# Optimization experiments

Hardware: AMD Instinct MI355X
Metric: run time of the kernel (lower is better)

The kernel has to match this reference:

```python
import jax, jax.numpy as jnp
import numpy as np

LATENT_DIM = 256
BOOK_SIZE = 8192


def setup_inputs() -> dict:
    key = jax.random.key(0)
    k1, k2 = jax.random.split(key)
    z_e = jax.random.normal(k1, (16, LATENT_DIM, 32, 32), dtype=jnp.float32)
    codebook = jax.random.normal(k2, (BOOK_SIZE, LATENT_DIM), dtype=jnp.float32)
    return {"z_e": z_e, "codebook": codebook}


def reference(z_e, codebook):
    # NCHW -> NHWC -> (B*H*W, D)
    flat_z = jnp.transpose(z_e, (0, 2, 3, 1)).reshape(-1, LATENT_DIM)
    # squared euclidean distance via matmul: ||z||^2 + ||e||^2 - 2 z.e
    dist = (
        jnp.sum(flat_z ** 2, axis=1, keepdims=True)
        + jnp.sum(codebook ** 2, axis=1)
        - 2.0 * flat_z @ codebook.T
    )  # (N, book_size)
    indices = jnp.argmin(dist, axis=1)          # (N,)
    z_q = codebook[indices]                      # (N, D) gather
    return z_q, indices
```

## Files before the change

### kernel.cpp

```cpp
#include <hip/hip_runtime.h>
#include <stdint.h>

#define NROWS 16384
#define NCODES 8192
#define DIM 256
#define EPS_S 0.4f
#define SM 0.5f

typedef __attribute__((ext_vector_type(8))) short bf16x8;
typedef __attribute__((ext_vector_type(16))) float f32x16;
typedef unsigned int uint32;

__device__ __forceinline__ unsigned short f2bf(float f) {
  union { float f; unsigned int u; } v; v.f = f;
  unsigned int u = v.u;
  return (unsigned short)((u + 0x7FFFu + ((u >> 16) & 1u)) >> 16);
}

__device__ __forceinline__ unsigned long long packdi(float d, int idx) {
  unsigned int u = __float_as_uint(d);
  u = (u & 0x80000000u) ? ~u : (u | 0x80000000u);
  return ((unsigned long long)u << 32) | (unsigned int)idx;
}
__device__ __forceinline__ unsigned long long u64min(unsigned long long a,
                                                     unsigned long long b) {
  return a < b ? a : b;
}
__device__ __forceinline__ unsigned long long shflx64(unsigned long long v, int m) {
  int lo = __shfl_xor((int)(unsigned int)v, m);
  int hi = __shfl_xor((int)(v >> 32), m);
  return ((unsigned long long)(unsigned int)hi << 32) | (unsigned int)lo;
}
__device__ __forceinline__ uint32 umax(uint32 a, uint32 b) { return a > b ? a : b; }
__device__ __forceinline__ uint32 umin(uint32 a, uint32 b) { return a < b ? a : b; }

__device__ __forceinline__ void glds16(const ushort* g, ushort* l) {
  __builtin_amdgcn_global_load_lds(
      (const __attribute__((address_space(1))) unsigned int*)g,
      (__attribute__((address_space(3))) unsigned int*)l, 16, 0, 0);
}

__global__ __launch_bounds__(256) void prep(const float* __restrict__ z,
                                            const float* __restrict__ cb,
                                            float* __restrict__ flatz,
                                            ushort* __restrict__ zb,
                                            ushort* __restrict__ eb,
                                            float* __restrict__ enorm) {
  __shared__ float t[32][33];
  const int blk = blockIdx.x;
  if (blk < 4096) {
    const int tx = threadIdx.x & 31, ty = threadIdx.x >> 5;
    const int ht = blk & 31, ct = (blk >> 5) & 7, b = blk >> 8;
    const float* src = z + (size_t)b * 262144 + (size_t)(ct * 32) * 1024 + ht * 32;
#pragma unroll
    for (int i = 0; i < 4; ++i) {
      int c = ty + i * 8;
      t[c][tx] = src[c * 1024 + tx];
    }
    __syncthreads();
    const int r = threadIdx.x >> 3, q = threadIdx.x & 7;
    float4 vv;
    vv.x = t[q * 4 + 0][r];
    vv.y = t[q * 4 + 1][r];
    vv.z = t[q * 4 + 2][r];
    vv.w = t[q * 4 + 3][r];
    const int row = b * 1024 + ht * 32 + r;
    *(float4*)(flatz + (size_t)row * 256 + ct * 32 + q * 4) = vv;
    ushort4 o;
    o.x = f2bf(vv.x); o.y = f2bf(vv.y); o.z = f2bf(vv.z); o.w = f2bf(vv.w);
    *(ushort4*)(zb + (size_t)row * 256 + ct * 32 + q * 4) = o;
  } else {
    const int lane = threadIdx.x & 63, wave = threadIdx.x >> 6;
    const int code = (blk - 4096) * 4 + wave;
    float4 v = *(const float4*)(cb + (size_t)code * 256 + lane * 4);
    ushort4 o;
    o.x = f2bf(v.x); o.y = f2bf(v.y); o.z = f2bf(v.z); o.w = f2bf(v.w);
    *(ushort4*)(eb + (size_t)code * 256 + lane * 4) = o;
    float ss = v.x * v.x + v.y * v.y + v.z * v.z + v.w * v.w;
#pragma unroll
    for (int s = 1; s < 64; s <<= 1) ss += __shfl_xor(ss, s);
    if (lane == 0) enorm[code] = ss;
  }
}

__device__ __forceinline__ void init_acc(f32x16 acc[4][2], const float* en,
                                         int ot, int wm, int lg) {
#pragma unroll
  for (int m = 0; m < 4; ++m) {
    const float* ep = en + ot * 256 + wm * 128 + m * 32 + 4 * lg;
    float4 e0 = *(const float4*)(ep);
    float4 e1 = *(const float4*)(ep + 8);
    float4 e2 = *(const float4*)(ep + 16);
    float4 e3 = *(const float4*)(ep + 24);
    f32x16 c0;
    c0[0]  = 1024.f - 0.5f * e0.x; c0[1]  = 1024.f - 0.5f * e0.y;
    c0[2]  = 1024.f - 0.5f * e0.z; c0[3]  = 1024.f - 0.5f * e0.w;
    c0[4]  = 1024.f - 0.5f * e1.x; c0[5]  = 1024.f - 0.5f * e1.y;
    c0[6]  = 1024.f - 0.5f * e1.z; c0[7]  = 1024.f - 0.5f * e1.w;
    c0[8]  = 1024.f - 0.5f * e2.x; c0[9]  = 1024.f - 0.5f * e2.y;
    c0[10] = 1024.f - 0.5f * e2.z; c0[11] = 1024.f - 0.5f * e2.w;
    c0[12] = 1024.f - 0.5f * e3.x; c0[13] = 1024.f - 0.5f * e3.y;
    c0[14] = 1024.f - 0.5f * e3.z; c0[15] = 1024.f - 0.5f * e3.w;
    acc[m][0] = c0; acc[m][1] = c0;
  }
}

__device__ __forceinline__ void epilogue(const f32x16 acc[4][2],
                                         uint32* __restrict__ bm, int cg,
                                         int ot, int zrow0, int wm, int wn,
                                         int l31, int lg) {
  const int cid0 = cg * 128 + ot * 16 + wm * 8;
#pragma unroll
  for (int n = 0; n < 2; ++n) {
    uint32 res[8];
#pragma unroll
    for (int m = 0; m < 4; ++m)
#pragma unroll
      for (int hc = 0; hc < 2; ++hc) {
        uint32 m1 = 0, m2 = 0;
#pragma unroll
        for (int p = 0; p < 8; ++p) {
          uint32 id = (uint32)((p & 3) | (lg << 2) | ((p >> 2) << 3));
          uint32 pv = (__float_as_uint(acc[m][n][hc * 8 + p]) & ~31u) | id;
          m2 = umax(m2, umin(m1, pv));
          m1 = umax(m1, pv);
        }
        uint32 o1 = (uint32)__shfl_xor((int)m1, 32);
        uint32 o2 = (uint32)__shfl_xor((int)m2, 32);
        m2 = umax(umax(m2, o2), umin(m1, o1));
        m1 = umax(m1, o1);
        float s1 = __uint_as_float(m1 & ~31u);
        float s2 = __uint_as_float(m2 & ~31u);
        res[m * 2 + hc] = (s1 - s2 > SM) ? (m1 | 16u) : m1;
      }
    const int zr = zrow0 + wn * 64 + n * 32 + l31;
    uint4 o;
    o.x = lg ? res[4] : res[0];
    o.y = lg ? res[5] : res[1];
    o.z = lg ? res[6] : res[2];
    o.w = lg ? res[7] : res[3];
    *(uint4*)(bm + (size_t)zr * 512 + cid0 + lg * 4) = o;
  }
}

__global__ __launch_bounds__(512, 2) void vq_gemm(const ushort* __restrict__ eb,
                                                  const ushort* __restrict__ zb,
                                                  const float* __restrict__ enorm,
                                                  uint32* __restrict__ bm) {
  __shared__ __align__(16) ushort As[4 * 8192];
  __shared__ __align__(16) ushort Bs[4 * 8192];
  __shared__ __align__(16) float en[2048];
  const int tid = threadIdx.x;
  const int wave = tid >> 6, lane = tid & 63;
  const int wm = wave >> 2, wn = wave & 3;
  const int l31 = lane & 31, lg = lane >> 5;
  const int y = blockIdx.x & 63, cg = blockIdx.x >> 6;
  const int code00 = cg * 2048;
  const int zrow0 = y * 256;

  *(float4*)&en[tid * 4] = *(const float4*)(enorm + code00 + tid * 4);
  __syncthreads();

  const int u0 = tid, u1 = tid + 512;
  const ushort* aU0 = eb + (size_t)(code00 + (u0 >> 2)) * 256 +
                      ((u0 & 3) ^ ((u0 >> 3) & 3)) * 8;
  const ushort* aU1 = eb + (size_t)(code00 + (u1 >> 2)) * 256 +
                      ((u1 & 3) ^ ((u1 >> 3) & 3)) * 8;
  const ushort* bU0 = zb + (size_t)(zrow0 + (u0 >> 2)) * 256 +
                      ((u0 & 3) ^ ((u0 >> 3) & 3)) * 8;
  const ushort* bU1 = zb + (size_t)(zrow0 + (u1 >> 2)) * 256 +
                      ((u1 & 3) ^ ((u1 >> 3) & 3)) * 8;
  ushort* aL = As + wave * 512;
  ushort* bL = Bs + wave * 512;

#pragma unroll
  for (int c = 0; c < 3; ++c) {
    glds16(aU0 + c * 32, aL + c * 8192);
    glds16(aU1 + c * 32, aL + c * 8192 + 4096);
    glds16(bU0 + c * 32, bL + c * 8192);
    glds16(bU1 + c * 32, bL + c * 8192 + 4096);
  }

  f32x16 acc[4][2];
  init_acc(acc, en, 0, wm, lg);

  asm volatile("s_waitcnt vmcnt(8)" ::: "memory");
  __builtin_amdgcn_s_barrier();
  asm volatile("" ::: "memory");

  const int swz = (l31 >> 1) & 3;
  const int colu0 = ((0 | lg) ^ swz) * 8;
  const int colu1 = ((2 | lg) ^ swz) * 8;
  const int arow_u = (wm * 128 + l31) * 32;
  const int brow_u = (wn * 64 + l31) * 32;

#pragma unroll 1
  for (int ot = 0; ot < 8; ++ot) {
    if (ot > 0) {
      epilogue(acc, bm, cg, ot - 1, zrow0, wm, wn, l31, lg);
      init_acc(acc, en, ot, wm, lg);
    }
#pragma unroll
    for (int cc = 0; cc < 8; ++cc) {
      const int slot = cc & 3;
      if (ot < 7 || cc <= 4) {
        const int s2 = (cc + 3) & 3;
        const size_t off = (size_t)((cc + 3) >> 3) * 65536 +
                           (size_t)ot * 65536 + ((cc + 3) & 7) * 32;
        const size_t boff = ((cc + 3) & 7) * 32;
        glds16(aU0 + off, aL + s2 * 8192);
        glds16(aU1 + off, aL + s2 * 8192 + 4096);
        glds16(bU0 + boff, bL + s2 * 8192);
        glds16(bU1 + boff, bL + s2 * 8192 + 4096);
      }
      bf16x8 a0[4], a1[4], b0[2], b1[2];
#pragma unroll
      for (int m = 0; m < 4; ++m) {
        a0[m] = *(const bf16x8*)&As[slot * 8192 + arow_u + m * 1024 + colu0];
        a1[m] = *(const bf16x8*)&As[slot * 8192 + arow_u + m * 1024 + colu1];
      }
#pragma unroll
      for (int n = 0; n < 2; ++n) {
        b0[n] = *(const bf16x8*)&Bs[slot * 8192 + brow_u + n * 1024 + colu0];
        b1[n] = *(const bf16x8*)&Bs[slot * 8192 + brow_u + n * 1024 + colu1];
      }
      __builtin_amdgcn_s_setprio(1);
#pragma unroll
      for (int m = 0; m < 4; ++m)
#pragma unroll
        for (int n = 0; n < 2; ++n)
          acc[m][n] = __builtin_amdgcn_mfma_f32_32x32x16_bf16(a0[m], b0[n],
                                                              acc[m][n], 0, 0, 0);
#pragma unroll
      for (int m = 0; m < 4; ++m)
#pragma unroll
        for (int n = 0; n < 2; ++n)
          acc[m][n] = __builtin_amdgcn_mfma_f32_32x32x16_bf16(a1[m], b1[n],
                                                              acc[m][n], 0, 0, 0);
      __builtin_amdgcn_s_setprio(0);
      if (ot < 7 || cc <= 4) {
        asm volatile("s_waitcnt vmcnt(8)" ::: "memory");
        __builtin_amdgcn_s_barrier();
        asm volatile("" ::: "memory");
      } else if (cc == 5) {
        asm volatile("s_waitcnt vmcnt(4)" ::: "memory");
        __builtin_amdgcn_s_barrier();
        asm volatile("" ::: "memory");
      } else if (cc == 6) {
        asm volatile("s_waitcnt vmcnt(0)" ::: "memory");
        __builtin_amdgcn_s_barrier();
        asm volatile("" ::: "memory");
      }
    }
  }
  epilogue(acc, bm, cg, 7, zrow0, wm, wn, l31, lg);
}

__device__ __forceinline__ unsigned long long chunk_exact(
    int chunk, const float* __restrict__ zrow, const float* __restrict__ cb,
    const float* __restrict__ enorm, int lane) {
  const int code = chunk * 16 + (lane >> 2);
  const float* zp = zrow + (lane & 3) * 64;
  const float* cp = cb + (size_t)code * 256 + (lane & 3) * 64;
  float s = 0.f;
#pragma unroll
  for (int d = 0; d < 64; d += 4) {
    float4 zv = *(const float4*)(zp + d);
    float4 cv = *(const float4*)(cp + d);
    s = fmaf(zv.x, cv.x, s); s = fmaf(zv.y, cv.y, s);
    s = fmaf(zv.z, cv.z, s); s = fmaf(zv.w, cv.w, s);
  }
  s += __shfl_xor(s, 1);
  s += __shfl_xor(s, 2);
  float dist = fmaf(-2.f, s, enorm[code]);
  unsigned long long key = ((lane & 3) == 0) ? packdi(dist, code) : ~0ull;
#pragma unroll
  for (int m = 1; m < 64; m <<= 1) key = u64min(key, shflx64(key, m));
  return key;
}

__global__ __launch_bounds__(256) void vq_sel(const uint32* __restrict__ bm,
                                              const float* __restrict__ flatz,
                                              const float* __restrict__ cb,
                                              const float* __restrict__ enorm,
                                              float* __restrict__ zq,
                                              float* __restrict__ oidx) {
  const int lane = threadIdx.x & 63;
  const int row = blockIdx.x * 4 + (threadIdx.x >> 6);
  uint4 va = *(const uint4*)(bm + (size_t)row * 512 + lane * 8);
  uint4 vb = *(const uint4*)(bm + (size_t)row * 512 + lane * 8 + 4);
  uint32 v[8] = {va.x, va.y, va.z, va.w, vb.x, vb.y, vb.z, vb.w};
  uint32 m1 = 0, m2 = 0; int ch = 0;
#pragma unroll
  for (int s = 0; s < 8; ++s) {
    uint32 pv = v[s];
    m2 = umax(m2, umin(m1, pv));
    ch = (pv > m1) ? (lane * 8 + s) : ch;
    m1 = umax(m1, pv);
  }
#pragma unroll
  for (int m = 1; m < 64; m <<= 1) {
    uint32 o1 = (uint32)__shfl_xor((int)m1, m);
    uint32 o2 = (uint32)__shfl_xor((int)m2, m);
    int oc = __shfl_xor(ch, m);
    m2 = umax(umax(m2, o2), umin(m1, o1));
    ch = (o1 > m1) ? oc : ch;
    m1 = umax(m1, o1);
  }
  float s1 = __uint_as_float(m1 & ~31u);
  float s2 = __uint_as_float(m2 & ~31u);
  int idx;
  if ((m1 & 16u) && (s1 - s2 > SM)) {
    idx = ch * 16 + (int)(m1 & 15u);
  } else {
    const float* zrow = flatz + (size_t)row * 256;
    unsigned long long key = chunk_exact(ch, zrow, cb, enorm, lane);
    float dbest;
    { unsigned int u = (unsigned int)(key >> 32);
      u = (u & 0x80000000u) ? (u & 0x7FFFFFFFu) : ~u;
      dbest = __uint_as_float(u); }
    float thr = (1024.f - 0.5f * dbest) - EPS_S;
#pragma unroll
    for (int s = 0; s < 8; ++s) {
      bool cand = __uint_as_float(v[s] & ~31u) >= thr;
      unsigned long long mk = __ballot(cand);
      while (mk) {
        int L = __ffsll(mk) - 1;
        mk &= mk - 1;
        int c2 = L * 8 + s;
        if (c2 == ch) continue;
        key = u64min(key, chunk_exact(c2, zrow, cb, enorm, lane));
      }
    }
    idx = (int)(key & 0xFFFFFFFFull);
  }
  if (lane == 0) oidx[row] = (float)idx;
  float4 val = *(const float4*)(cb + (size_t)idx * 256 + lane * 4);
  *(float4*)(zq + (size_t)row * 256 + lane * 4) = val;
}

extern "C" void kernel_launch(void* const* d_in, const int* in_sizes, int n_in,
                              void* d_out, int out_size, void* d_ws, size_t ws_size,
                              hipStream_t stream) {
  const float* z = (const float*)d_in[0];
  const float* cb = (const float*)d_in[1];
  char* ws = (char*)d_ws;
  ushort* zb = (ushort*)(ws);
  ushort* eb = (ushort*)(ws + (8u << 20));
  float* enorm = (float*)(ws + (12u << 20));
  uint32* bm = (uint32*)(ws + (13u << 20));
  float* zq = (float*)d_out;
  float* oidx = zq + (size_t)NROWS * DIM;
  float* flatz = zq;

  prep<<<4096 + NCODES / 4, 256, 0, stream>>>(z, cb, flatz, zb, eb, enorm);
  vq_gemm<<<256, 512, 0, stream>>>(eb, zb, enorm, bm);
  vq_sel<<<NROWS / 4, 256, 0, stream>>>(bm, flatz, cb, enorm, zq, oidx);
}
```

Measured before the change: 181.7 us.

## Keep codebook tile resident in LDS and stream z rows instead

Restructures the GEMM block so each block loads a full 256-code by 256-dim codebook tile into shared memory once, with an XOR swizzle, and then streams 8 consecutive 256-row z tiles through a double-buffered LDS buffer. Previously each block kept z fixed and streamed codebook chunks through a 4-stage ring. The aim is to cut repeated global codebook traffic and the per-block enorm staging. The cost is a 2-stage pipeline that waits on vmcnt(0) every chunk, so load latency is exposed more, and a different grid mapping.

```diff
diff --git a/kernel.cpp b/kernel.cpp
--- a/kernel.cpp
+++ b/kernel.cpp
@@ -83,11 +83,12 @@
   }
 }
 
-__device__ __forceinline__ void init_acc(f32x16 acc[4][2], const float* en,
-                                         int ot, int wm, int lg) {
+__device__ __forceinline__ void init_acc(f32x16 acc[4][2],
+                                         const float* __restrict__ epb,
+                                         int wm, int lg) {
 #pragma unroll
   for (int m = 0; m < 4; ++m) {
-    const float* ep = en + ot * 256 + wm * 128 + m * 32 + 4 * lg;
+    const float* ep = epb + wm * 128 + m * 32 + 4 * lg;
     float4 e0 = *(const float4*)(ep);
     float4 e1 = *(const float4*)(ep + 8);
     float4 e2 = *(const float4*)(ep + 16);
@@ -106,10 +107,10 @@
 }
 
 __device__ __forceinline__ void epilogue(const f32x16 acc[4][2],
-                                         uint32* __restrict__ bm, int cg,
-                                         int ot, int zrow0, int wm, int wn,
+                                         uint32* __restrict__ bm, int cid0b,
+                                         int zrowb, int wm, int wn,
                                          int l31, int lg) {
-  const int cid0 = cg * 128 + ot * 16 + wm * 8;
+  const int cid0 = cid0b + wm * 8;
 #pragma unroll
   for (int n = 0; n < 2; ++n) {
     uint32 res[8];
@@ -133,7 +134,7 @@
         float s2 = __uint_as_float(m2 & ~31u);
         res[m * 2 + hc] = (s1 - s2 > SM) ? (m1 | 16u) : m1;
       }
-    const int zr = zrow0 + wn * 64 + n * 32 + l31;
+    const int zr = zrowb + wn * 64 + n * 32 + l31;
     uint4 o;
     o.x = lg ? res[4] : res[0];
     o.y = lg ? res[5] : res[1];
@@ -147,82 +148,77 @@
                                                   const ushort* __restrict__ zb,
                                                   const float* __restrict__ enorm,
                                                   uint32* __restrict__ bm) {
-  __shared__ __align__(16) ushort As[4 * 8192];
-  __shared__ __align__(16) ushort Bs[4 * 8192];
-  __shared__ __align__(16) float en[2048];
+  __shared__ __align__(16) ushort Am[65536];
+  __shared__ __align__(16) ushort Bsr[16384];
   const int tid = threadIdx.x;
   const int wave = tid >> 6, lane = tid & 63;
   const int wm = wave >> 2, wn = wave & 3;
   const int l31 = lane & 31, lg = lane >> 5;
-  const int y = blockIdx.x & 63, cg = blockIdx.x >> 6;
-  const int code00 = cg * 2048;
-  const int zrow0 = y * 256;
-
-  *(float4*)&en[tid * 4] = *(const float4*)(enorm + code00 + tid * 4);
+  const int cg = blockIdx.x & 31, yg = blockIdx.x >> 5;
+  const int code0 = cg * 256;
+  const int zrow00 = yg * 2048;
+  const int cid0b = cg * 16;
+
+#pragma unroll
+  for (int j = 0; j < 16; ++j) {
+    const int u = tid + j * 512;
+    const int row = u >> 5;
+    const int g = (u & 31) ^ (row & 7);
+    glds16(eb + (size_t)(code0 + row) * 256 + g * 8,
+           Am + (wave * 64 + j * 512) * 8);
+  }
+
+  const int u0 = tid, u1 = tid + 512;
+  const ushort* bU0 = zb + (size_t)(zrow00 + (u0 >> 2)) * 256 +
+                      ((u0 & 3) ^ ((u0 >> 3) & 3)) * 8;
+  const ushort* bU1 = zb + (size_t)(zrow00 + (u1 >> 2)) * 256 +
+                      ((u1 & 3) ^ ((u1 >> 3) & 3)) * 8;
+  ushort* bL = Bsr + wave * 512;
+
+  glds16(bU0, bL);
+  glds16(bU1, bL + 4096);
+
+  asm volatile("s_waitcnt vmcnt(0)" ::: "memory");
   __syncthreads();
 
-  const int u0 = tid, u1 = tid + 512;
-  const ushort* aU0 = eb + (size_t)(code00 + (u0 >> 2)) * 256 +
-                      ((u0 & 3) ^ ((u0 >> 3) & 3)) * 8;
-  const ushort* aU1 = eb + (size_t)(code00 + (u1 >> 2)) * 256 +
-                      ((u1 & 3) ^ ((u1 >> 3) & 3)) * 8;
-  const ushort* bU0 = zb + (size_t)(zrow0 + (u0 >> 2)) * 256 +
-                      ((u0 & 3) ^ ((u0 >> 3) & 3)) * 8;
-  const ushort* bU1 = zb + (size_t)(zrow0 + (u1 >> 2)) * 256 +
-                      ((u1 & 3) ^ ((u1 >> 3) & 3)) * 8;
-  ushort* aL = As + wave * 512;
-  ushort* bL = Bs + wave * 512;
-
-#pragma unroll
-  for (int c = 0; c < 3; ++c) {
-    glds16(aU0 + c * 32, aL + c * 8192);
-    glds16(aU1 + c * 32, aL + c * 8192 + 4096);
-    glds16(bU0 + c * 32, bL + c * 8192);
-    glds16(bU1 + c * 32, bL + c * 8192 + 4096);
-  }
-
   f32x16 acc[4][2];
-  init_acc(acc, en, 0, wm, lg);
-
-  asm volatile("s_waitcnt vmcnt(8)" ::: "memory");
-  __builtin_amdgcn_s_barrier();
-  asm volatile("" ::: "memory");
-
-  const int swz = (l31 >> 1) & 3;
-  const int colu0 = ((0 | lg) ^ swz) * 8;
-  const int colu1 = ((2 | lg) ^ swz) * 8;
-  const int arow_u = (wm * 128 + l31) * 32;
+  init_acc(acc, enorm + code0, wm, lg);
+
+  const int swzA = l31 & 7;
+  const int arow = (wm * 128 + l31) * 256;
+  const int swzB = (l31 >> 1) & 3;
+  const int colu0 = ((0 | lg) ^ swzB) * 8;
+  const int colu1 = ((2 | lg) ^ swzB) * 8;
   const int brow_u = (wn * 64 + l31) * 32;
 
 #pragma unroll 1
-  for (int ot = 0; ot < 8; ++ot) {
-    if (ot > 0) {
-      epilogue(acc, bm, cg, ot - 1, zrow0, wm, wn, l31, lg);
-      init_acc(acc, en, ot, wm, lg);
+  for (int yp = 0; yp < 8; ++yp) {
+    if (yp > 0) {
+      epilogue(acc, bm, cid0b, zrow00 + (yp - 1) * 256, wm, wn, l31, lg);
+      init_acc(acc, enorm + code0, wm, lg);
     }
 #pragma unroll
-    for (int cc = 0; cc < 8; ++cc) {
-      const int slot = cc & 3;
-      if (ot < 7 || cc <= 4) {
-        const int s2 = (cc + 3) & 3;
-        const size_t off = (size_t)((cc + 3) >> 3) * 65536 +
-                           (size_t)ot * 65536 + ((cc + 3) & 7) * 32;
-        const size_t boff = ((cc + 3) & 7) * 32;
-        glds16(aU0 + off, aL + s2 * 8192);
-        glds16(aU1 + off, aL + s2 * 8192 + 4096);
-        glds16(bU0 + boff, bL + s2 * 8192);
-        glds16(bU1 + boff, bL + s2 * 8192 + 4096);
+    for (int kc = 0; kc < 8; ++kc) {
+      const int c = yp * 8 + kc;
+      const int slot = c & 1;
+      if (c < 63) {
+        const int cn = c + 1;
+        const size_t off = (size_t)(cn >> 3) * 65536 + (size_t)(cn & 7) * 32;
+        glds16(bU0 + off, bL + (slot ^ 1) * 8192);
+        glds16(bU1 + off, bL + (slot ^ 1) * 8192 + 4096);
       }
       bf16x8 a0[4], a1[4], b0[2], b1[2];
 #pragma unroll
       for (int m = 0; m < 4; ++m) {
-        a0[m] = *(const bf16x8*)&As[slot * 8192 + arow_u + m * 1024 + colu0];
-        a1[m] = *(const bf16x8*)&As[slot * 8192 + arow_u + m * 1024 + colu1];
+        a0[m] = *(const bf16x8*)&Am[arow + m * 8192 +
+                                    (((kc * 4 + 0) | lg) ^ swzA) * 8];
+        a1[m] = *(const bf16x8*)&Am[arow + m * 8192 +
+                                    (((kc * 4 + 2) | lg) ^ swzA) * 8];
       }
 #pragma unroll
       for (int n = 0; n < 2; ++n) {
-        b0[n] = *(const bf16x8*)&Bs[slot * 8192 + brow_u + n * 1024 + colu0];
-        b1[n] = *(const bf16x8*)&Bs[slot * 8192 + brow_u + n * 1024 + colu1];
+        b0[n] = *(const bf16x8*)&Bsr[slot * 8192 + brow_u + n * 1024 + colu0];
+        b1[n] = *(const bf16x8*)&Bsr[slot * 8192 + brow_u + n * 1024 + colu1];
       }
       __builtin_amdgcn_s_setprio(1);
 #pragma unroll
@@ -238,22 +234,14 @@
           acc[m][n] = __builtin_amdgcn_mfma_f32_32x32x16_bf16(a1[m], b1[n],
                                                               acc[m][n], 0, 0, 0);
       __builtin_amdgcn_s_setprio(0);
-      if (ot < 7 || cc <= 4) {
-        asm volatile("s_waitcnt vmcnt(8)" ::: "memory");
-        __builtin_amdgcn_s_barrier();
-        asm volatile("" ::: "memory");
-      } else if (cc == 5) {
-        asm volatile("s_waitcnt vmcnt(4)" ::: "memory");
-        __builtin_amdgcn_s_barrier();
-        asm volatile("" ::: "memory");
-      } else if (cc == 6) {
+      if (c < 63) {
         asm volatile("s_waitcnt vmcnt(0)" ::: "memory");
         __builtin_amdgcn_s_barrier();
         asm volatile("" ::: "memory");
       }
     }
   }
-  epilogue(acc, bm, cg, 7, zrow0, wm, wn, l31, lg);
+  epilogue(acc, bm, cid0b, zrow00 + 7 * 256, wm, wn, l31, lg);
 }
 
 __device__ __forceinline__ unsigned long long chunk_exact(
```

Measured after the change: 177.3 us. 1.02x faster.
